# Kernel optimization log

Measured on AMD Instinct MI355X. Metric: run time of the kernel, lower is better.

Reference implementation:

```python
import jax, jax.numpy as jnp
import numpy as np

EPS = 1e-10
LOSS_COEF = 0.01

def cv_squared(v):
    # torch .var() is unbiased (ddof=1)
    return jnp.var(v, ddof=1) / (jnp.mean(v) ** 2 + EPS)

def setup_inputs() -> dict:
    B, Q, D, H, O, E = 4096, 256, 512, 1024, 512, 16
    key = jax.random.key(0)
    ks = jax.random.split(key, 8)
    return {
        "query": jax.random.normal(ks[0], (B, Q), jnp.float32),
        "x": jax.random.normal(ks[1], (B, D), jnp.float32),
        "w_gate": jax.random.normal(ks[2], (D, E), jnp.float32) * 0.02,
        "task_gate": jax.random.normal(ks[3], (Q, E), jnp.float32) * 0.02,
        "W1": jax.random.normal(ks[4], (E, D, H), jnp.float32) * 0.02,
        "b1": jnp.zeros((E, H), jnp.float32),
        "W2": jax.random.normal(ks[5], (E, H, O), jnp.float32) * 0.02,
        "b2": jnp.zeros((E, O), jnp.float32),
        "k": 4,
    }

def reference(query, x, w_gate, task_gate, W1, b1, W2, b2, k):
    B = x.shape[0]
    E = w_gate.shape[1]
    # --- top-k gating (eval mode: clean logits, no noise) ---
    logits = x @ w_gate + query @ task_gate                      # [B, E]
    m = min(k + 1, E)
    top_vals, top_idx = jax.lax.top_k(logits, m)                 # [B, m]
    topk_gates = jax.nn.softmax(top_vals[:, :k], axis=1)         # [B, k]
    rows = jnp.arange(B)[:, None]
    gates = jnp.zeros_like(logits).at[rows, top_idx[:, :k]].set(topk_gates)  # [B, E]
    importance = gates.sum(0)                                    # [E]
    load = (gates > 0).sum(0).astype(jnp.float32)                # [E]
    loss = LOSS_COEF * (cv_squared(importance) + cv_squared(load))
    # --- dispatch / expert MLP / combine ---
    # gate==0 contributions vanish, so weighting by gates is exactly
    # equivalent to the sparse gather -> expert -> index_add combine.
    y = jnp.zeros((B, W2.shape[2]), jnp.float32)
    for e in range(E):  # fixed small loop over experts
        h = jax.nn.relu(x @ W1[e] + b1[e])                       # [B, H]
        out = h @ W2[e] + b2[e]                                  # [B, O]
        y = y + gates[:, e:e + 1] * out
    return y, loss
```

## Files before the change

kernel.cpp:

```cpp
#include <hip/hip_runtime.h>

typedef short bf16x8_t __attribute__((ext_vector_type(8)));
typedef short bf16x4_t __attribute__((ext_vector_type(4)));
typedef float f32x4_t __attribute__((ext_vector_type(4)));

#define B_DIM 4096
#define Q_DIM 256
#define D_DIM 512
#define H_DIM 1024
#define O_DIM 512
#define E_NUM 16
#define K_TOP 4

#define BM 128
#define BN 128
#define BK 32

__device__ __forceinline__ short f2bf(float f) {
  unsigned int u = __float_as_uint(f);
  u += 0x7FFFu + ((u >> 16) & 1u);
  return (short)(u >> 16);
}

__device__ __forceinline__ void g2l16(const void* g, void* l) {
  __builtin_amdgcn_global_load_lds(
      (const __attribute__((address_space(1))) void*)(unsigned long long)(size_t)g,
      (__attribute__((address_space(3))) void*)(unsigned)(size_t)l, 16, 0, 0);
}

__device__ __forceinline__ void tr_tile(float (*tile)[65], const float* __restrict__ s,
                                        short* __restrict__ d, int R, int C, int r0, int c0,
                                        int t) {
#pragma unroll
  for (int i = 0; i < 16; i++) {
    int lin = i * 256 + t;
    int rr = lin >> 6, cc = lin & 63;
    tile[rr][cc] = s[(size_t)(r0 + rr) * C + (c0 + cc)];
  }
  __syncthreads();
#pragma unroll
  for (int i = 0; i < 2; i++) {
    int task = i * 256 + t;
    int cr = task >> 3, g = task & 7;
    bf16x8_t v;
#pragma unroll
    for (int j = 0; j < 8; j++) v[j] = f2bf(tile[g * 8 + j][cr]);
    *(bf16x8_t*)(d + (size_t)(c0 + cr) * R + r0 + g * 8) = v;
  }
}

__global__ __launch_bounds__(256) void weights_prep(
    const float* __restrict__ W1, const float* __restrict__ W2,
    const float* __restrict__ wg, const float* __restrict__ tg,
    short* __restrict__ w1t, short* __restrict__ w2t, float* __restrict__ wpack) {
  __shared__ float tile[64][65];
  const int blk = blockIdx.x, t = threadIdx.x;
  if (blk < 2048) {
    int e = blk >> 7, rem = blk & 127;
    int r0 = (rem >> 4) * 64, c0 = (rem & 15) * 64;
    tr_tile(tile, W1 + (size_t)e * D_DIM * H_DIM, w1t + (size_t)e * D_DIM * H_DIM,
            D_DIM, H_DIM, r0, c0, t);
  } else if (blk < 4096) {
    int b2 = blk - 2048;
    int e = b2 >> 7, rem = b2 & 127;
    int r0 = (rem >> 3) * 64, c0 = (rem & 7) * 64;
    tr_tile(tile, W2 + (size_t)e * H_DIM * O_DIM, w2t + (size_t)e * H_DIM * O_DIM,
            H_DIM, O_DIM, r0, c0, t);
  } else {
    int lin = (blk - 4096) * 256 + t;
    if (lin < E_NUM * 768) {
      int e = lin / 768, r = lin % 768;
      wpack[lin] = (r < D_DIM) ? wg[r * E_NUM + e] : tg[(r - D_DIM) * E_NUM + e];
    }
  }
}

__global__ __launch_bounds__(256) void gating_kernel(
    const float* __restrict__ x, const float* __restrict__ query,
    const float* __restrict__ wpack,
    int4* __restrict__ topk_e4, float4* __restrict__ topk_g4, short* __restrict__ x_bf) {
  __shared__ __align__(16) float4 s_w[E_NUM * 192];
  const int t = threadIdx.x, wv = t >> 6, lane = t & 63;
  const float4* wp4 = (const float4*)wpack;
#pragma unroll
  for (int i = 0; i < 12; i++) s_w[i * 256 + t] = wp4[i * 256 + t];
  __syncthreads();

  const int row = blockIdx.x * 4 + wv;
  const float4* xr = (const float4*)(x + (size_t)row * D_DIM);
  const float4* qr = (const float4*)(query + (size_t)row * Q_DIM);
  const float4 xv0 = xr[lane], xv1 = xr[64 + lane], qv = qr[lane];

  {
    bf16x4_t v0, v1;
    v0[0] = f2bf(xv0.x); v0[1] = f2bf(xv0.y); v0[2] = f2bf(xv0.z); v0[3] = f2bf(xv0.w);
    v1[0] = f2bf(xv1.x); v1[1] = f2bf(xv1.y); v1[2] = f2bf(xv1.z); v1[3] = f2bf(xv1.w);
    short* xb = x_bf + (size_t)row * D_DIM;
    *(bf16x4_t*)(xb + lane * 4) = v0;
    *(bf16x4_t*)(xb + 256 + lane * 4) = v1;
  }

  float p[E_NUM];
#pragma unroll
  for (int e = 0; e < E_NUM; e++) {
    float4 w0 = s_w[e * 192 + lane];
    float4 w1 = s_w[e * 192 + 64 + lane];
    float4 wq = s_w[e * 192 + 128 + lane];
    p[e] = xv0.x * w0.x + xv0.y * w0.y + xv0.z * w0.z + xv0.w * w0.w +
           xv1.x * w1.x + xv1.y * w1.y + xv1.z * w1.z + xv1.w * w1.w +
           qv.x * wq.x + qv.y * wq.y + qv.z * wq.z + qv.w * wq.w;
  }
#pragma unroll
  for (int e = 0; e < E_NUM; e++) {
    p[e] += __shfl_xor(p[e], 16, 64);
    p[e] += __shfl_xor(p[e], 32, 64);
  }
#pragma unroll
  for (int s = 8; s >= 1; s >>= 1) {
    const bool take = (lane & s) != 0;
#pragma unroll
    for (int j = 0; j < s; j++) {
      float keep = take ? p[j + s] : p[j];
      float send = take ? p[j] : p[j + s];
      p[j] = keep + __shfl_xor(send, s, 64);
    }
  }
  const float logit = p[0];
  float v[E_NUM];
#pragma unroll
  for (int i = 0; i < E_NUM; i++) v[i] = __shfl(logit, i, 64);

  if (lane == 0) {
    int idx[K_TOP];
    float val[K_TOP];
    unsigned used = 0;
    for (int k = 0; k < K_TOP; k++) {
      float best = -3.4e38f;
      int bi = 0;
      for (int i = 0; i < E_NUM; i++)
        if (!(used & (1u << i)) && v[i] > best) { best = v[i]; bi = i; }
      used |= 1u << bi;
      idx[k] = bi;
      val[k] = best;
    }
    float mx = val[0];
    float ex[K_TOP], Z = 0.f;
    for (int k = 0; k < K_TOP; k++) { ex[k] = __expf(val[k] - mx); Z += ex[k]; }
    topk_e4[row] = make_int4(idx[0], idx[1], idx[2], idx[3]);
    topk_g4[row] = make_float4(ex[0] / Z, ex[1] / Z, ex[2] / Z, ex[3] / Z);
  }
}

__global__ __launch_bounds__(256) void csr_kernel(
    const int4* __restrict__ topk_e4, const float4* __restrict__ topk_g4,
    int* __restrict__ count, float* __restrict__ imp_g,
    int* __restrict__ rowlist, int* __restrict__ slotid, float* __restrict__ egate) {
  const int e = blockIdx.x, t = threadIdx.x;
  __shared__ int s_cnt[256];
  __shared__ float s_gs[64];
  int c = 0;
  float gs = 0.f;
#pragma unroll 4
  for (int i = 0; i < 16; i++) {
    int row = t * 16 + i;
    int4 v = topk_e4[row];
    float4 g = topk_g4[row];
    if (v.x == e) { c++; gs += g.x; }
    if (v.y == e) { c++; gs += g.y; }
    if (v.z == e) { c++; gs += g.z; }
    if (v.w == e) { c++; gs += g.w; }
  }
  s_cnt[t] = c;
  float gw = gs;
  for (int off = 32; off >= 1; off >>= 1) gw += __shfl_down(gw, off, 64);
  if ((t & 63) == 0) s_gs[t >> 6] = gw;
  __syncthreads();
  for (int off = 1; off < 256; off <<= 1) {
    int vv = (t >= off) ? s_cnt[t - off] : 0;
    __syncthreads();
    s_cnt[t] += vv;
    __syncthreads();
  }
  int pos = s_cnt[t] - c;
#pragma unroll 4
  for (int i = 0; i < 16; i++) {
    int row = t * 16 + i;
    int4 v = topk_e4[row];
    float4 g = topk_g4[row];
    int ve[4] = {v.x, v.y, v.z, v.w};
    float vg[4] = {g.x, g.y, g.z, g.w};
#pragma unroll
    for (int k = 0; k < K_TOP; k++) {
      if (ve[k] == e) {
        rowlist[e * B_DIM + pos] = row;
        slotid[e * B_DIM + pos] = row * K_TOP + k;
        egate[e * B_DIM + pos] = vg[k];
        pos++;
      }
    }
  }
  if (t == 0) {
    count[e] = s_cnt[255];
    imp_g[e] = s_gs[0] + s_gs[1] + s_gs[2] + s_gs[3];
  }
}

__global__ __launch_bounds__(64) void loss_offsets_kernel(
    const int* __restrict__ count, const float* __restrict__ imp_g,
    int* __restrict__ offs, float* __restrict__ out_loss) {
  if (threadIdx.x == 0) {
    float mi = 0.f, ml = 0.f;
    for (int i = 0; i < E_NUM; i++) { mi += imp_g[i]; ml += (float)count[i]; }
    mi /= (float)E_NUM;
    ml /= (float)E_NUM;
    float vi = 0.f, vl = 0.f;
    for (int i = 0; i < E_NUM; i++) {
      float di = imp_g[i] - mi;
      vi += di * di;
      float dl = (float)count[i] - ml;
      vl += dl * dl;
    }
    vi /= (float)(E_NUM - 1);
    vl /= (float)(E_NUM - 1);
    out_loss[0] = 0.01f * (vi / (mi * mi + 1e-10f) + vl / (ml * ml + 1e-10f));
    int run = 0;
    for (int i = 0; i < E_NUM; i++) { offs[i] = run; run += count[i]; }
  }
}

__global__ __launch_bounds__(256) void gemm1_kernel(
    const short* __restrict__ x_bf, const short* __restrict__ w1t,
    const float* __restrict__ b1, const int* __restrict__ count,
    const int* __restrict__ offs, const int* __restrict__ rowlist,
    short* __restrict__ h_buf) {
  const int flat = blockIdx.x;
  const int xcd = flat & 7, j = flat >> 3;
  const int mt = j & 31, gidx = j >> 5;
  const int group = xcd * 16 + gidx;
  const int e = group >> 3, nt = group & 7;
  const int n_e = count[e];
  if (mt * BM >= n_e) return;
  __shared__ __align__(16) short As[BM * BK];
  __shared__ __align__(16) short Bs[BN * BK];
  const int t = threadIdx.x, lane = t & 63, wv = t >> 6;
  const int wm = wv >> 1, wn = wv & 1;
  const int srow = wv * 16 + (lane >> 2);
  const int kb = (lane & 3) * 8;
  int gr0 = mt * BM + srow;       gr0 = gr0 < n_e ? gr0 : n_e - 1;
  int gr1 = mt * BM + 64 + srow;  gr1 = gr1 < n_e ? gr1 : n_e - 1;
  const short* pa0 = x_bf + (size_t)rowlist[e * B_DIM + gr0] * D_DIM + kb;
  const short* pa1 = x_bf + (size_t)rowlist[e * B_DIM + gr1] * D_DIM + kb;
  const short* w1te = w1t + ((size_t)e * H_DIM + nt * BN) * D_DIM;
  const short* pb0 = w1te + (size_t)srow * D_DIM + kb;
  const short* pb1 = w1te + (size_t)(64 + srow) * D_DIM + kb;
  short* lA0 = As + wv * 16 * BK;
  short* lA1 = As + (64 + wv * 16) * BK;
  short* lB0 = Bs + wv * 16 * BK;
  short* lB1 = Bs + (64 + wv * 16) * BK;

  f32x4_t acc[4][4] = {};
  const int frow = lane & 15, kg = lane >> 4;

  for (int k0 = 0; k0 < D_DIM; k0 += BK) {
    g2l16(pa0 + k0, lA0);
    g2l16(pa1 + k0, lA1);
    g2l16(pb0 + k0, lB0);
    g2l16(pb1 + k0, lB1);
    __syncthreads();
    bf16x8_t af[4], bfr[4];
#pragma unroll
    for (int mi = 0; mi < 4; mi++)
      af[mi] = *(const bf16x8_t*)&As[(wm * 64 + mi * 16 + frow) * BK + kg * 8];
#pragma unroll
    for (int ni = 0; ni < 4; ni++)
      bfr[ni] = *(const bf16x8_t*)&Bs[(wn * 64 + ni * 16 + frow) * BK + kg * 8];
#pragma unroll
    for (int mi = 0; mi < 4; mi++)
#pragma unroll
      for (int ni = 0; ni < 4; ni++)
        acc[mi][ni] = __builtin_amdgcn_mfma_f32_16x16x32_bf16(af[mi], bfr[ni], acc[mi][ni], 0, 0, 0);
    __syncthreads();
  }
  const int obase = offs[e];
#pragma unroll
  for (int mi = 0; mi < 4; mi++) {
#pragma unroll
    for (int r = 0; r < 4; r++) {
      int row = wm * 64 + mi * 16 + kg * 4 + r;
      int m_local = mt * BM + row;
      if (m_local >= n_e) continue;
      size_t hrow = (size_t)(obase + m_local) * H_DIM;
#pragma unroll
      for (int ni = 0; ni < 4; ni++) {
        int col = nt * BN + wn * 64 + ni * 16 + frow;
        float vv = acc[mi][ni][r] + b1[e * H_DIM + col];
        h_buf[hrow + col] = f2bf(vv > 0.f ? vv : 0.f);
      }
    }
  }
}

__global__ __launch_bounds__(256) void gemm2_kernel(
    const short* __restrict__ h_buf, const short* __restrict__ w2t,
    const float* __restrict__ b2, const int* __restrict__ count,
    const int* __restrict__ offs, const int* __restrict__ slotid,
    const float* __restrict__ egate, float* __restrict__ out_buf) {
  const int flat = blockIdx.x;
  const int xcd = flat & 7, j = flat >> 3;
  const int nt = j & 3, gidx = j >> 2;
  const int group = xcd * 64 + gidx;
  const int e = group >> 5, mt = group & 31;
  const int n_e = count[e];
  if (mt * BM >= n_e) return;
  __shared__ __align__(16) short As[BM * BK];
  __shared__ __align__(16) short Bs[BN * BK];
  const int t = threadIdx.x, lane = t & 63, wv = t >> 6;
  const int wm = wv >> 1, wn = wv & 1;
  const int srow = wv * 16 + (lane >> 2);
  const int kb = (lane & 3) * 8;
  const int obase = offs[e];
  int gr0 = mt * BM + srow;       gr0 = gr0 < n_e ? gr0 : n_e - 1;
  int gr1 = mt * BM + 64 + srow;  gr1 = gr1 < n_e ? gr1 : n_e - 1;
  const short* pa0 = h_buf + (size_t)(obase + gr0) * H_DIM + kb;
  const short* pa1 = h_buf + (size_t)(obase + gr1) * H_DIM + kb;
  const short* w2te = w2t + ((size_t)e * O_DIM + nt * BN) * H_DIM;
  const short* pb0 = w2te + (size_t)srow * H_DIM + kb;
  const short* pb1 = w2te + (size_t)(64 + srow) * H_DIM + kb;
  short* lA0 = As + wv * 16 * BK;
  short* lA1 = As + (64 + wv * 16) * BK;
  short* lB0 = Bs + wv * 16 * BK;
  short* lB1 = Bs + (64 + wv * 16) * BK;

  f32x4_t acc[4][4] = {};
  const int frow = lane & 15, kg = lane >> 4;

  for (int k0 = 0; k0 < H_DIM; k0 += BK) {
    g2l16(pa0 + k0, lA0);
    g2l16(pa1 + k0, lA1);
    g2l16(pb0 + k0, lB0);
    g2l16(pb1 + k0, lB1);
    __syncthreads();
    bf16x8_t af[4], bfr[4];
#pragma unroll
    for (int mi = 0; mi < 4; mi++)
      af[mi] = *(const bf16x8_t*)&As[(wm * 64 + mi * 16 + frow) * BK + kg * 8];
#pragma unroll
    for (int ni = 0; ni < 4; ni++)
      bfr[ni] = *(const bf16x8_t*)&Bs[(wn * 64 + ni * 16 + frow) * BK + kg * 8];
#pragma unroll
    for (int mi = 0; mi < 4; mi++)
#pragma unroll
      for (int ni = 0; ni < 4; ni++)
        acc[mi][ni] = __builtin_amdgcn_mfma_f32_16x16x32_bf16(af[mi], bfr[ni], acc[mi][ni], 0, 0, 0);
    __syncthreads();
  }
#pragma unroll
  for (int mi = 0; mi < 4; mi++) {
#pragma unroll
    for (int r = 0; r < 4; r++) {
      int row = wm * 64 + mi * 16 + kg * 4 + r;
      int m_local = mt * BM + row;
      if (m_local >= n_e) continue;
      float g = egate[e * B_DIM + m_local];
      size_t orow = (size_t)slotid[e * B_DIM + m_local] * O_DIM;
#pragma unroll
      for (int ni = 0; ni < 4; ni++) {
        int col = nt * BN + wn * 64 + ni * 16 + frow;
        out_buf[orow + col] = (acc[mi][ni][r] + b2[e * O_DIM + col]) * g;
      }
    }
  }
}

__global__ __launch_bounds__(256) void combine_kernel(const float* __restrict__ out_buf,
                                                      float* __restrict__ y) {
  int idx = blockIdx.x * 256 + threadIdx.x;
  int b = idx >> 7;
  int o = (idx & 127) << 2;
  const float* base = out_buf + (size_t)b * K_TOP * O_DIM + o;
  float4 a0 = *(const float4*)(base);
  float4 a1 = *(const float4*)(base + O_DIM);
  float4 a2 = *(const float4*)(base + 2 * O_DIM);
  float4 a3 = *(const float4*)(base + 3 * O_DIM);
  float4 r;
  r.x = a0.x + a1.x + a2.x + a3.x;
  r.y = a0.y + a1.y + a2.y + a3.y;
  r.z = a0.z + a1.z + a2.z + a3.z;
  r.w = a0.w + a1.w + a2.w + a3.w;
  *(float4*)(y + (size_t)b * O_DIM + o) = r;
}

extern "C" void kernel_launch(void* const* d_in, const int* in_sizes, int n_in,
                              void* d_out, int out_size, void* d_ws, size_t ws_size,
                              hipStream_t stream) {
  (void)in_sizes; (void)n_in; (void)out_size; (void)ws_size;
  const float* query = (const float*)d_in[0];
  const float* x = (const float*)d_in[1];
  const float* wg = (const float*)d_in[2];
  const float* tg = (const float*)d_in[3];
  const float* W1 = (const float*)d_in[4];
  const float* b1 = (const float*)d_in[5];
  const float* W2 = (const float*)d_in[6];
  const float* b2 = (const float*)d_in[7];
  float* y = (float*)d_out;

  char* ws = (char*)d_ws;
  int* count = (int*)(ws + 0);
  float* imp = (float*)(ws + 64);
  int* offs = (int*)(ws + 128);
  int* rowlist = (int*)(ws + 256);
  int* slotid = (int*)(ws + 262400);
  float* egate = (float*)(ws + 524544);
  int4* topk_e4 = (int4*)(ws + 786688);
  float4* topk_g4 = (float4*)(ws + 852224);
  float* wpack = (float*)(ws + 917760);
  short* h_buf = (short*)(ws + 1048576);
  short* w2t = (short*)(ws + 34603008);
  short* x_bf = (short*)(ws + 51380224);
  short* w1t = (short*)(ws + 55574528);
  float* out_buf = (float*)(ws + 51380224);

  weights_prep<<<dim3(4144), 256, 0, stream>>>(W1, W2, wg, tg, w1t, w2t, wpack);
  gating_kernel<<<dim3(B_DIM / 4), 256, 0, stream>>>(x, query, wpack, topk_e4, topk_g4, x_bf);
  csr_kernel<<<dim3(E_NUM), 256, 0, stream>>>(topk_e4, topk_g4, count, imp,
                                              rowlist, slotid, egate);
  loss_offsets_kernel<<<1, 64, 0, stream>>>(count, imp, offs, y + (size_t)B_DIM * O_DIM);
  gemm1_kernel<<<dim3(4096), 256, 0, stream>>>(x_bf, w1t, b1, count, offs, rowlist, h_buf);
  gemm2_kernel<<<dim3(2048), 256, 0, stream>>>(h_buf, w2t, b2, count, offs, slotid, egate,
                                               out_buf);
  combine_kernel<<<dim3(B_DIM * O_DIM / 4 / 256), 256, 0, stream>>>(out_buf, y);
}
```

Measured before the change: 235.8 us.

## Fuse weight prep with gating and double the K-step in expert GEMMs

Merges the weight-transpose kernel and the gating kernel into one launch, with each gating block building its own transposed gate-weight table in shared memory instead of reading a separately packed buffer. Both expert GEMMs now load two BK slices per barrier pair, halving the number of __syncthreads in the K loop at the cost of doubled LDS use. The loss/offsets kernel stages counts in shared memory first. Every gating block redoes the gate-weight transpose, and the larger LDS footprint may lower GEMM occupancy.

```diff
diff --git a/kernel.cpp b/kernel.cpp
--- a/kernel.cpp
+++ b/kernel.cpp
@@ -49,44 +49,57 @@
   }
 }
 
-__global__ __launch_bounds__(256) void weights_prep(
+__global__ __launch_bounds__(256) void prep_gate_kernel(
+    const float* __restrict__ x, const float* __restrict__ query,
+    const float* __restrict__ wg, const float* __restrict__ tg,
     const float* __restrict__ W1, const float* __restrict__ W2,
-    const float* __restrict__ wg, const float* __restrict__ tg,
-    short* __restrict__ w1t, short* __restrict__ w2t, float* __restrict__ wpack) {
-  __shared__ float tile[64][65];
+    short* __restrict__ w1t, short* __restrict__ w2t, short* __restrict__ x_bf,
+    int4* __restrict__ topk_e4, float4* __restrict__ topk_g4) {
+  __shared__ __align__(16) float smem[12288];
   const int blk = blockIdx.x, t = threadIdx.x;
-  if (blk < 2048) {
-    int e = blk >> 7, rem = blk & 127;
-    int r0 = (rem >> 4) * 64, c0 = (rem & 15) * 64;
-    tr_tile(tile, W1 + (size_t)e * D_DIM * H_DIM, w1t + (size_t)e * D_DIM * H_DIM,
-            D_DIM, H_DIM, r0, c0, t);
-  } else if (blk < 4096) {
-    int b2 = blk - 2048;
-    int e = b2 >> 7, rem = b2 & 127;
-    int r0 = (rem >> 3) * 64, c0 = (rem & 7) * 64;
-    tr_tile(tile, W2 + (size_t)e * H_DIM * O_DIM, w2t + (size_t)e * H_DIM * O_DIM,
-            H_DIM, O_DIM, r0, c0, t);
-  } else {
-    int lin = (blk - 4096) * 256 + t;
-    if (lin < E_NUM * 768) {
-      int e = lin / 768, r = lin % 768;
-      wpack[lin] = (r < D_DIM) ? wg[r * E_NUM + e] : tg[(r - D_DIM) * E_NUM + e];
-    }
-  }
-}
-
-__global__ __launch_bounds__(256) void gating_kernel(
-    const float* __restrict__ x, const float* __restrict__ query,
-    const float* __restrict__ wpack,
-    int4* __restrict__ topk_e4, float4* __restrict__ topk_g4, short* __restrict__ x_bf) {
-  __shared__ __align__(16) float4 s_w[E_NUM * 192];
-  const int t = threadIdx.x, wv = t >> 6, lane = t & 63;
-  const float4* wp4 = (const float4*)wpack;
-#pragma unroll
-  for (int i = 0; i < 12; i++) s_w[i * 256 + t] = wp4[i * 256 + t];
+
+  if (blk >= 1024) {
+    float(*tile)[65] = (float(*)[65])smem;
+    if (blk < 3072) {
+      int b = blk - 1024;
+      int e = b >> 7, rem = b & 127;
+      int r0 = (rem >> 4) * 64, c0 = (rem & 15) * 64;
+      tr_tile(tile, W1 + (size_t)e * D_DIM * H_DIM, w1t + (size_t)e * D_DIM * H_DIM,
+              D_DIM, H_DIM, r0, c0, t);
+    } else {
+      int b = blk - 3072;
+      int e = b >> 7, rem = b & 127;
+      int r0 = (rem >> 3) * 64, c0 = (rem & 7) * 64;
+      tr_tile(tile, W2 + (size_t)e * H_DIM * O_DIM, w2t + (size_t)e * H_DIM * O_DIM,
+              H_DIM, O_DIM, r0, c0, t);
+    }
+    return;
+  }
+
+#pragma unroll
+  for (int i = 0; i < 12; i++) {
+    int idx4 = (i * 256 + t) * 4;
+    if (idx4 < D_DIM * E_NUM) {
+      float4 v = *(const float4*)(wg + idx4);
+      int d = idx4 >> 4, e0 = idx4 & 15;
+      smem[(e0 + 0) * 768 + d] = v.x;
+      smem[(e0 + 1) * 768 + d] = v.y;
+      smem[(e0 + 2) * 768 + d] = v.z;
+      smem[(e0 + 3) * 768 + d] = v.w;
+    } else {
+      int l2 = idx4 - D_DIM * E_NUM;
+      float4 v = *(const float4*)(tg + l2);
+      int q = l2 >> 4, e0 = l2 & 15;
+      smem[(e0 + 0) * 768 + 512 + q] = v.x;
+      smem[(e0 + 1) * 768 + 512 + q] = v.y;
+      smem[(e0 + 2) * 768 + 512 + q] = v.z;
+      smem[(e0 + 3) * 768 + 512 + q] = v.w;
+    }
+  }
   __syncthreads();
 
-  const int row = blockIdx.x * 4 + wv;
+  const int wv = t >> 6, lane = t & 63;
+  const int row = blk * 4 + wv;
   const float4* xr = (const float4*)(x + (size_t)row * D_DIM);
   const float4* qr = (const float4*)(query + (size_t)row * Q_DIM);
   const float4 xv0 = xr[lane], xv1 = xr[64 + lane], qv = qr[lane];
@@ -100,12 +113,13 @@
     *(bf16x4_t*)(xb + 256 + lane * 4) = v1;
   }
 
+  const float4* s_w4 = (const float4*)smem;
   float p[E_NUM];
 #pragma unroll
   for (int e = 0; e < E_NUM; e++) {
-    float4 w0 = s_w[e * 192 + lane];
-    float4 w1 = s_w[e * 192 + 64 + lane];
-    float4 wq = s_w[e * 192 + 128 + lane];
+    float4 w0 = s_w4[e * 192 + lane];
+    float4 w1 = s_w4[e * 192 + 64 + lane];
+    float4 wq = s_w4[e * 192 + 128 + lane];
     p[e] = xv0.x * w0.x + xv0.y * w0.y + xv0.z * w0.z + xv0.w * w0.w +
            xv1.x * w1.x + xv1.y * w1.y + xv1.z * w1.z + xv1.w * w1.w +
            qv.x * wq.x + qv.y * wq.y + qv.z * wq.z + qv.w * wq.w;
@@ -208,23 +222,28 @@
 __global__ __launch_bounds__(64) void loss_offsets_kernel(
     const int* __restrict__ count, const float* __restrict__ imp_g,
     int* __restrict__ offs, float* __restrict__ out_loss) {
-  if (threadIdx.x == 0) {
+  __shared__ int s_c[E_NUM];
+  __shared__ float s_i[E_NUM];
+  const int t = threadIdx.x;
+  if (t < E_NUM) { s_c[t] = count[t]; s_i[t] = imp_g[t]; }
+  __syncthreads();
+  if (t == 0) {
     float mi = 0.f, ml = 0.f;
-    for (int i = 0; i < E_NUM; i++) { mi += imp_g[i]; ml += (float)count[i]; }
+    for (int i = 0; i < E_NUM; i++) { mi += s_i[i]; ml += (float)s_c[i]; }
     mi /= (float)E_NUM;
     ml /= (float)E_NUM;
     float vi = 0.f, vl = 0.f;
     for (int i = 0; i < E_NUM; i++) {
-      float di = imp_g[i] - mi;
+      float di = s_i[i] - mi;
       vi += di * di;
-      float dl = (float)count[i] - ml;
+      float dl = (float)s_c[i] - ml;
       vl += dl * dl;
     }
     vi /= (float)(E_NUM - 1);
     vl /= (float)(E_NUM - 1);
     out_loss[0] = 0.01f * (vi / (mi * mi + 1e-10f) + vl / (ml * ml + 1e-10f));
     int run = 0;
-    for (int i = 0; i < E_NUM; i++) { offs[i] = run; run += count[i]; }
+    for (int i = 0; i < E_NUM; i++) { offs[i] = run; run += s_c[i]; }
   }
 }
 
@@ -240,8 +259,8 @@
   const int e = group >> 3, nt = group & 7;
   const int n_e = count[e];
   if (mt * BM >= n_e) return;
-  __shared__ __align__(16) short As[BM * BK];
-  __shared__ __align__(16) short Bs[BN * BK];
+  __shared__ __align__(16) short As0[BM * BK], As1[BM * BK];
+  __shared__ __align__(16) short Bs0[BN * BK], Bs1[BN * BK];
   const int t = threadIdx.x, lane = t & 63, wv = t >> 6;
   const int wm = wv >> 1, wn = wv & 1;
   const int srow = wv * 16 + (lane >> 2);
@@ -253,32 +272,39 @@
   const short* w1te = w1t + ((size_t)e * H_DIM + nt * BN) * D_DIM;
   const short* pb0 = w1te + (size_t)srow * D_DIM + kb;
   const short* pb1 = w1te + (size_t)(64 + srow) * D_DIM + kb;
-  short* lA0 = As + wv * 16 * BK;
-  short* lA1 = As + (64 + wv * 16) * BK;
-  short* lB0 = Bs + wv * 16 * BK;
-  short* lB1 = Bs + (64 + wv * 16) * BK;
+  const int lo0 = wv * 16 * BK, lo1 = (64 + wv * 16) * BK;
 
   f32x4_t acc[4][4] = {};
   const int frow = lane & 15, kg = lane >> 4;
 
-  for (int k0 = 0; k0 < D_DIM; k0 += BK) {
-    g2l16(pa0 + k0, lA0);
-    g2l16(pa1 + k0, lA1);
-    g2l16(pb0 + k0, lB0);
-    g2l16(pb1 + k0, lB1);
-    __syncthreads();
-    bf16x8_t af[4], bfr[4];
-#pragma unroll
-    for (int mi = 0; mi < 4; mi++)
-      af[mi] = *(const bf16x8_t*)&As[(wm * 64 + mi * 16 + frow) * BK + kg * 8];
-#pragma unroll
-    for (int ni = 0; ni < 4; ni++)
-      bfr[ni] = *(const bf16x8_t*)&Bs[(wn * 64 + ni * 16 + frow) * BK + kg * 8];
-#pragma unroll
-    for (int mi = 0; mi < 4; mi++)
+  for (int k0 = 0; k0 < D_DIM; k0 += 2 * BK) {
+    g2l16(pa0 + k0, As0 + lo0);
+    g2l16(pa1 + k0, As0 + lo1);
+    g2l16(pb0 + k0, Bs0 + lo0);
+    g2l16(pb1 + k0, Bs0 + lo1);
+    g2l16(pa0 + k0 + BK, As1 + lo0);
+    g2l16(pa1 + k0 + BK, As1 + lo1);
+    g2l16(pb0 + k0 + BK, Bs1 + lo0);
+    g2l16(pb1 + k0 + BK, Bs1 + lo1);
+    __syncthreads();
+#pragma unroll
+    for (int half = 0; half < 2; half++) {
+      const short* A = half ? As1 : As0;
+      const short* B = half ? Bs1 : Bs0;
+      bf16x8_t af[4], bfr[4];
+#pragma unroll
+      for (int mi = 0; mi < 4; mi++)
+        af[mi] = *(const bf16x8_t*)&A[(wm * 64 + mi * 16 + frow) * BK + kg * 8];
 #pragma unroll
       for (int ni = 0; ni < 4; ni++)
-        acc[mi][ni] = __builtin_amdgcn_mfma_f32_16x16x32_bf16(af[mi], bfr[ni], acc[mi][ni], 0, 0, 0);
+        bfr[ni] = *(const bf16x8_t*)&B[(wn * 64 + ni * 16 + frow) * BK + kg * 8];
+#pragma unroll
+      for (int mi = 0; mi < 4; mi++)
+#pragma unroll
+        for (int ni = 0; ni < 4; ni++)
+          acc[mi][ni] =
+              __builtin_amdgcn_mfma_f32_16x16x32_bf16(af[mi], bfr[ni], acc[mi][ni], 0, 0, 0);
+    }
     __syncthreads();
   }
   const int obase = offs[e];
@@ -312,8 +338,8 @@
   const int e = group >> 5, mt = group & 31;
   const int n_e = count[e];
   if (mt * BM >= n_e) return;
-  __shared__ __align__(16) short As[BM * BK];
-  __shared__ __align__(16) short Bs[BN * BK];
+  __shared__ __align__(16) short As0[BM * BK], As1[BM * BK];
+  __shared__ __align__(16) short Bs0[BN * BK], Bs1[BN * BK];
   const int t = threadIdx.x, lane = t & 63, wv = t >> 6;
   const int wm = wv >> 1, wn = wv & 1;
   const int srow = wv * 16 + (lane >> 2);
@@ -326,32 +352,39 @@
   const short* w2te = w2t + ((size_t)e * O_DIM + nt * BN) * H_DIM;
   const short* pb0 = w2te + (size_t)srow * H_DIM + kb;
   const short* pb1 = w2te + (size_t)(64 + srow) * H_DIM + kb;
-  short* lA0 = As + wv * 16 * BK;
-  short* lA1 = As + (64 + wv * 16) * BK;
-  short* lB0 = Bs + wv * 16 * BK;
-  short* lB1 = Bs + (64 + wv * 16) * BK;
+  const int lo0 = wv * 16 * BK, lo1 = (64 + wv * 16) * BK;
 
   f32x4_t acc[4][4] = {};
   const int frow = lane & 15, kg = lane >> 4;
 
-  for (int k0 = 0; k0 < H_DIM; k0 += BK) {
-    g2l16(pa0 + k0, lA0);
-    g2l16(pa1 + k0, lA1);
-    g2l16(pb0 + k0, lB0);
-    g2l16(pb1 + k0, lB1);
-    __syncthreads();
-    bf16x8_t af[4], bfr[4];
-#pragma unroll
-    for (int mi = 0; mi < 4; mi++)
-      af[mi] = *(const bf16x8_t*)&As[(wm * 64 + mi * 16 + frow) * BK + kg * 8];
-#pragma unroll
-    for (int ni = 0; ni < 4; ni++)
-      bfr[ni] = *(const bf16x8_t*)&Bs[(wn * 64 + ni * 16 + frow) * BK + kg * 8];
-#pragma unroll
-    for (int mi = 0; mi < 4; mi++)
+  for (int k0 = 0; k0 < H_DIM; k0 += 2 * BK) {
+    g2l16(pa0 + k0, As0 + lo0);
+    g2l16(pa1 + k0, As0 + lo1);
+    g2l16(pb0 + k0, Bs0 + lo0);
+    g2l16(pb1 + k0, Bs0 + lo1);
+    g2l16(pa0 + k0 + BK, As1 + lo0);
+    g2l16(pa1 + k0 + BK, As1 + lo1);
+    g2l16(pb0 + k0 + BK, Bs1 + lo0);
+    g2l16(pb1 + k0 + BK, Bs1 + lo1);
+    __syncthreads();
+#pragma unroll
+    for (int half = 0; half < 2; half++) {
+      const short* A = half ? As1 : As0;
+      const short* B = half ? Bs1 : Bs0;
+      bf16x8_t af[4], bfr[4];
+#pragma unroll
+      for (int mi = 0; mi < 4; mi++)
+        af[mi] = *(const bf16x8_t*)&A[(wm * 64 + mi * 16 + frow) * BK + kg * 8];
 #pragma unroll
       for (int ni = 0; ni < 4; ni++)
-        acc[mi][ni] = __builtin_amdgcn_mfma_f32_16x16x32_bf16(af[mi], bfr[ni], acc[mi][ni], 0, 0, 0);
+        bfr[ni] = *(const bf16x8_t*)&B[(wn * 64 + ni * 16 + frow) * BK + kg * 8];
+#pragma unroll
+      for (int mi = 0; mi < 4; mi++)
+#pragma unroll
+        for (int ni = 0; ni < 4; ni++)
+          acc[mi][ni] =
+              __builtin_amdgcn_mfma_f32_16x16x32_bf16(af[mi], bfr[ni], acc[mi][ni], 0, 0, 0);
+    }
     __syncthreads();
   }
 #pragma unroll
@@ -413,15 +446,14 @@
   float* egate = (float*)(ws + 524544);
   int4* topk_e4 = (int4*)(ws + 786688);
   float4* topk_g4 = (float4*)(ws + 852224);
-  float* wpack = (float*)(ws + 917760);
   short* h_buf = (short*)(ws + 1048576);
   short* w2t = (short*)(ws + 34603008);
   short* x_bf = (short*)(ws + 51380224);
   short* w1t = (short*)(ws + 55574528);
   float* out_buf = (float*)(ws + 51380224);
 
-  weights_prep<<<dim3(4144), 256, 0, stream>>>(W1, W2, wg, tg, w1t, w2t, wpack);
-  gating_kernel<<<dim3(B_DIM / 4), 256, 0, stream>>>(x, query, wpack, topk_e4, topk_g4, x_bf);
+  prep_gate_kernel<<<dim3(5120), 256, 0, stream>>>(x, query, wg, tg, W1, W2,
+                                                   w1t, w2t, x_bf, topk_e4, topk_g4);
   csr_kernel<<<dim3(E_NUM), 256, 0, stream>>>(topk_e4, topk_g4, count, imp,
                                               rowlist, slotid, egate);
   loss_offsets_kernel<<<1, 64, 0, stream>>>(count, imp, offs, y + (size_t)B_DIM * O_DIM);
```

After: 249.4 us. 5.8% more time.
